# Kernel tuning notes

Hardware: AMD Instinct MI355X
Metric: run time of the kernel (lower is better)

The kernel has to match this reference:

```python
import jax, jax.numpy as jnp
import numpy as np
import math

D_MODEL = 1024
NUM_HEADS = 16
D_KV = 64
INNER = NUM_HEADS * D_KV
NUM_BUCKETS = 32
MAX_DISTANCE = 128


def _relative_position_bucket(relative_position, num_buckets=NUM_BUCKETS, max_distance=MAX_DISTANCE):
    # bidirectional T5 bucketing
    n = -relative_position
    num_buckets = num_buckets // 2
    ret = (n < 0).astype(jnp.int32) * num_buckets
    n = jnp.abs(n)
    max_exact = num_buckets // 2
    is_small = n < max_exact
    n_safe = jnp.maximum(n, 1).astype(jnp.float32)  # avoid log(0); masked by is_small
    val_if_large = max_exact + (
        jnp.log(n_safe / max_exact) / math.log(max_distance / max_exact) * (num_buckets - max_exact)
    ).astype(jnp.int32)
    val_if_large = jnp.minimum(val_if_large, num_buckets - 1)
    return jnp.where(is_small, n, val_if_large) + ret


def _position_bias(rel_emb, q_len, k_len):
    ctx = jnp.arange(q_len)[:, None]
    mem = jnp.arange(k_len)[None, :]
    buckets = _relative_position_bucket(mem - ctx)          # [q, k]
    values = rel_emb[buckets]                               # [q, k, H]
    return jnp.transpose(values, (2, 0, 1))[None]           # [1, H, q, k]


def setup_inputs() -> dict:
    key = jax.random.key(0)
    ks = jax.random.split(key, 6)
    B, S = 2, 2048
    scale = 1.0 / math.sqrt(D_MODEL)
    return {
        "hidden_states": jax.random.normal(ks[0], (B, S, D_MODEL), dtype=jnp.float32),
        "mask": jnp.zeros((B, 1, 1, S), dtype=jnp.float32),
        "Wq": jax.random.normal(ks[1], (D_MODEL, INNER), dtype=jnp.float32) * scale,
        "Wk": jax.random.normal(ks[2], (D_MODEL, INNER), dtype=jnp.float32) * scale,
        "Wv": jax.random.normal(ks[3], (D_MODEL, INNER), dtype=jnp.float32) * scale,
        "Wo": jax.random.normal(ks[4], (INNER, D_MODEL), dtype=jnp.float32) * scale,
        "rel_emb": jax.random.normal(ks[5], (NUM_BUCKETS, NUM_HEADS), dtype=jnp.float32),
    }


def reference(hidden_states, mask, Wq, Wk, Wv, Wo, rel_emb):
    B, S, _ = hidden_states.shape
    def split_heads(x):
        return jnp.transpose(x.reshape(B, -1, NUM_HEADS, D_KV), (0, 2, 1, 3))  # [B,H,S,d]
    q = split_heads(hidden_states @ Wq)
    k = split_heads(hidden_states @ Wk)
    v = split_heads(hidden_states @ Wv)
    scores = jnp.einsum("bhqd,bhkd->bhqk", q, k)            # unscaled, T5-style
    position_bias = _position_bias(rel_emb, S, S)           # [1,H,S,S]
    scores = scores + position_bias + mask
    attn = jax.nn.softmax(scores, axis=-1)
    context = jnp.einsum("bhqk,bhkd->bhqd", attn, v)
    context = jnp.transpose(context, (0, 2, 1, 3)).reshape(B, S, INNER)
    output = context @ Wo
    return output, position_bias
```

## Files before the change

kernel.cpp:

```cpp
#include <hip/hip_runtime.h>
#include <cstdint>

#define AS1 __attribute__((address_space(1)))
#define AS3 __attribute__((address_space(3)))

typedef _Float16 half8 __attribute__((ext_vector_type(8)));
typedef _Float16 half4_t __attribute__((ext_vector_type(4)));
typedef float v4f __attribute__((ext_vector_type(4)));

__device__ __forceinline__ void async_ld16(const void* g, void* l) {
  __builtin_amdgcn_global_load_lds((const AS1 uint32_t*)g, (AS3 uint32_t*)l, 16, 0, 0);
}

__device__ __forceinline__ int t5_bucket(int delta) {
  int n = -delta;
  int ret = 0;
  if (n < 0) { ret = 16; n = -n; }
  if (n < 8) return n + ret;
  if (n >= 91) return 15 + ret;
  if ((n & (n - 1)) == 0) {
    int l = 31 - __clz(n);
    int v = 2 + 2 * l;
    return (v > 15 ? 15 : v) + ret;
  }
  int v = 8 + (int)(logf((float)n * 0.125f) * (8.0f / logf(16.0f)));
  return (v > 15 ? 15 : v) + ret;
}

__global__ void k_prep(const float* __restrict__ hs, const float* __restrict__ Wq,
                       const float* __restrict__ Wk, const float* __restrict__ Wv,
                       const float* __restrict__ Wo, _Float16* __restrict__ hsF,
                       _Float16* __restrict__ wqkvT, _Float16* __restrict__ woT) {
  const int tid = threadIdx.x;
  if (blockIdx.x < 4096) {
    int t = blockIdx.x * 256 + tid;
    float4 f = ((const float4*)hs)[t];
    half4_t h = {(_Float16)f.x, (_Float16)f.y, (_Float16)f.z, (_Float16)f.w};
    ((half4_t*)hsF)[t] = h;
    return;
  }
  __shared__ float tile[32][33];
  const int idx = blockIdx.x - 4096;
  const int z = idx >> 10, rem = idx & 1023;
  const float* src = (z == 0) ? Wq : (z == 1) ? Wk : (z == 2) ? Wv : Wo;
  _Float16* dst = (z < 3) ? (wqkvT + ((size_t)z << 20)) : woT;
  const int tx = tid & 31, ty = tid >> 5;
  const int bx = (rem & 31) * 32, by = (rem >> 5) * 32;
#pragma unroll
  for (int i = 0; i < 32; i += 8)
    tile[ty + i][tx] = src[(size_t)(by + ty + i) * 1024 + bx + tx];
  __syncthreads();
#pragma unroll
  for (int i = 0; i < 32; i += 8)
    dst[(size_t)(bx + ty + i) * 1024 + by + tx] = (_Float16)tile[tx][ty + i];
}

__global__ __launch_bounds__(256, 3) void k_gemm_qkv_bias(
    const _Float16* __restrict__ A, const _Float16* __restrict__ BT,
    _Float16* __restrict__ qkv, _Float16* __restrict__ vT,
    const float* __restrict__ rel, float* __restrict__ outb) {
  __shared__ __align__(16) _Float16 As[128 * 32];
  __shared__ __align__(16) _Float16 Bs[128 * 32];
  __shared__ float btab[256];
  const int tid = threadIdx.x;
  const int wave = tid >> 6, lane = tid & 63;
  const int l15 = lane & 15, quad = lane >> 4;
  const int m0 = blockIdx.y * 128, n0 = blockIdx.x * 128;
  const int wm = (wave >> 1) * 64, wn = (wave & 1) * 64;
  const int r0 = tid >> 2, c0 = (tid & 3) * 8;
  constexpr int K = 1024;

  const int bid = blockIdx.y * 24 + blockIdx.x;
  const bool do_bias = bid < 512;
  const int hB = bid >> 5;
  const int qoff = (bid & 31) * 64;
  float c_past = 0.f, c_fut = 0.f;
  if (do_bias) {
    btab[tid & 255] = rel[t5_bucket((tid & 255) - 128) * 16 + hB];
    c_past = rel[15 * 16 + hB];
    c_fut = rel[31 * 16 + hB];
  }

  v4f acc[4][4] = {};
  for (int k0 = 0; k0 < K; k0 += 32) {
    asm volatile("s_waitcnt lgkmcnt(0)\ns_barrier" ::: "memory");
    async_ld16(A + (size_t)(m0 + r0) * K + k0 + c0, (char*)As + (size_t)(wave * 64) * 16);
    async_ld16(A + (size_t)(m0 + 64 + r0) * K + k0 + c0,
               (char*)As + (size_t)(256 + wave * 64) * 16);
    async_ld16(BT + (size_t)(n0 + r0) * K + k0 + c0, (char*)Bs + (size_t)(wave * 64) * 16);
    async_ld16(BT + (size_t)(n0 + 64 + r0) * K + k0 + c0,
               (char*)Bs + (size_t)(256 + wave * 64) * 16);

    if (do_bias) {
      __builtin_amdgcn_sched_barrier(0);
      const int iter = k0 >> 5;
#pragma unroll
      for (int j = 0; j < 2; ++j) {
        int fi = iter * 512 + j * 256 + tid;
        int qr = qoff + (fi >> 8);
        int c = fi & 255;
        int k4 = ((c >> 4) << 5) + (c & 15);
        int kb = k4 << 2;
        float4 v;
        if (kb - qr >= 91) {
          v = make_float4(c_fut, c_fut, c_fut, c_fut);
        } else if (qr - kb - 3 >= 91) {
          v = make_float4(c_past, c_past, c_past, c_past);
        } else {
          v.x = btab[kb + 0 - qr + 128];
          v.y = btab[kb + 1 - qr + 128];
          v.z = btab[kb + 2 - qr + 128];
          v.w = btab[kb + 3 - qr + 128];
        }
        ((float4*)outb)[((size_t)hB * 2048 + qr) * 512 + k4] = v;
      }
      asm volatile("s_waitcnt vmcnt(2) lgkmcnt(0)\ns_barrier" ::: "memory");
    } else {
      asm volatile("s_waitcnt vmcnt(0) lgkmcnt(0)\ns_barrier" ::: "memory");
    }

    half8 af[4], bf[4];
#pragma unroll
    for (int mt = 0; mt < 4; ++mt)
      af[mt] = *(const half8*)(As + (wm + mt * 16 + l15) * 32 + quad * 8);
#pragma unroll
    for (int nt = 0; nt < 4; ++nt)
      bf[nt] = *(const half8*)(Bs + (wn + nt * 16 + l15) * 32 + quad * 8);
#pragma unroll
    for (int mt = 0; mt < 4; ++mt)
#pragma unroll
      for (int nt = 0; nt < 4; ++nt)
        acc[mt][nt] = __builtin_amdgcn_mfma_f32_16x16x32_f16(af[mt], bf[nt], acc[mt][nt], 0, 0, 0);
  }
  if (n0 >= 2048) {
#pragma unroll
    for (int mt = 0; mt < 4; ++mt)
#pragma unroll
      for (int nt = 0; nt < 4; ++nt) {
        int col = n0 + wn + nt * 16 + l15 - 2048;
        int row0 = m0 + wm + mt * 16 + quad * 4;
        int bb = row0 >> 11, s0 = row0 & 2047;
        half4_t hv = {(_Float16)acc[mt][nt][0], (_Float16)acc[mt][nt][1],
                      (_Float16)acc[mt][nt][2], (_Float16)acc[mt][nt][3]};
        *(half4_t*)(vT + ((size_t)bb * 1024 + col) * 2048 + s0) = hv;
      }
    return;
  }
#pragma unroll
  for (int mt = 0; mt < 4; ++mt)
#pragma unroll
    for (int nt = 0; nt < 4; ++nt)
#pragma unroll
      for (int r = 0; r < 4; ++r)
        qkv[(size_t)(m0 + wm + mt * 16 + quad * 4 + r) * 3072 + n0 + wn + nt * 16 + l15] =
            (_Float16)acc[mt][nt][r];
}

__global__ __launch_bounds__(256, 2) void k_gemm_n64(const _Float16* __restrict__ A,
                                                     const _Float16* __restrict__ BT,
                                                     float* __restrict__ C, int K, int ldc) {
  __shared__ __align__(16) _Float16 As[128 * 32];
  __shared__ __align__(16) _Float16 Bs[64 * 32];
  const int tid = threadIdx.x;
  const int wave = tid >> 6, lane = tid & 63;
  const int l15 = lane & 15, quad = lane >> 4;
  const int m0 = blockIdx.y * 128, n0 = blockIdx.x * 64;
  const int wm = (wave >> 1) * 64, wn = (wave & 1) * 32;
  const int r0 = tid >> 2, c0 = (tid & 3) * 8;
  v4f acc[4][2] = {};
  for (int k0 = 0; k0 < K; k0 += 32) {
    asm volatile("s_waitcnt lgkmcnt(0)\ns_barrier" ::: "memory");
    async_ld16(A + (size_t)(m0 + r0) * K + k0 + c0, (char*)As + (size_t)(wave * 64) * 16);
    async_ld16(A + (size_t)(m0 + 64 + r0) * K + k0 + c0,
               (char*)As + (size_t)(256 + wave * 64) * 16);
    async_ld16(BT + (size_t)(n0 + r0) * K + k0 + c0, (char*)Bs + (size_t)(wave * 64) * 16);
    asm volatile("s_waitcnt vmcnt(0) lgkmcnt(0)\ns_barrier" ::: "memory");
    half8 af[4], bf[2];
#pragma unroll
    for (int mt = 0; mt < 4; ++mt)
      af[mt] = *(const half8*)(As + (wm + mt * 16 + l15) * 32 + quad * 8);
#pragma unroll
    for (int nt = 0; nt < 2; ++nt)
      bf[nt] = *(const half8*)(Bs + (wn + nt * 16 + l15) * 32 + quad * 8);
#pragma unroll
    for (int mt = 0; mt < 4; ++mt)
#pragma unroll
      for (int nt = 0; nt < 2; ++nt)
        acc[mt][nt] = __builtin_amdgcn_mfma_f32_16x16x32_f16(af[mt], bf[nt], acc[mt][nt], 0, 0, 0);
  }
#pragma unroll
  for (int mt = 0; mt < 4; ++mt)
#pragma unroll
    for (int nt = 0; nt < 2; ++nt)
#pragma unroll
      for (int r = 0; r < 4; ++r)
        C[(size_t)(m0 + wm + mt * 16 + quad * 4 + r) * ldc + n0 + wn + nt * 16 + l15] =
            acc[mt][nt][r];
}

__global__ __launch_bounds__(512, 4) void k_attn(const _Float16* __restrict__ qkv,
                                                 const _Float16* __restrict__ vT,
                                                 const float* __restrict__ mask,
                                                 const float* __restrict__ rel,
                                                 _Float16* __restrict__ ctx,
                                                 float* __restrict__ outb) {
  constexpr int S = 2048, LD = 3072;
  __shared__ __align__(16) _Float16 Ks[2][64 * 72];
  __shared__ __align__(16) _Float16 VT[2][64 * 72];
  __shared__ __align__(16) _Float16 Psh[128 * 72];
  __shared__ float btab[512];
  const int tid = threadIdx.x, wave = tid >> 6, lane = tid & 63;
  const int l15 = lane & 15, quad = lane >> 4;
  const int flat = blockIdx.x + 16 * (blockIdx.y + 16 * blockIdx.z);
  const int swz = (flat & 7) * 64 + (flat >> 3);
  const int q0 = (swz & 15) * 128, h = (swz >> 4) & 15, b = swz >> 8;

  btab[tid] = rel[t5_bucket((int)tid - 256) * 16 + h];
  const float c_past = rel[15 * 16 + h];
  const float c_fut = rel[31 * 16 + h];

  half8 bq[2];
  {
    const _Float16* qp = qkv + (size_t)(b * S + q0 + wave * 16 + l15) * LD + h * 64;
    bq[0] = *(const half8*)(qp + quad * 8);
    bq[1] = *(const half8*)(qp + 32 + quad * 8);
  }
  v4f o[4] = {};
  float mrun = -INFINITY;
  float lrun = 0.f;

  const int srow = tid >> 3, scol = (tid & 7) * 8;
  const _Float16* kg = qkv + (size_t)(b * S + srow) * LD + 1024 + h * 64 + scol;
  const _Float16* vg = vT + ((size_t)((b * 16 + h) * 64 + srow)) * S + scol;
  const float4* mkp = (const float4*)(mask + (size_t)b * S);

  const int qrow0 = q0 + b * 64;
  float4* const bias_base = (float4*)outb + ((size_t)h * 2048 + qrow0) * 512;

  {
    half8 kr = *(const half8*)(kg);
    half8 vr = *(const half8*)(vg);
    *(half8*)(&Ks[0][srow * 72 + scol]) = kr;
    *(half8*)(&VT[0][srow * 72 + scol]) = vr;
  }
  float4 mk[4];
#pragma unroll
  for (int mt = 0; mt < 4; ++mt) mk[mt] = mkp[mt * 4 + quad];
  __syncthreads();

  for (int kv0 = 0; kv0 < S; kv0 += 64) {
    const int buf = (kv0 >> 6) & 1;
    const bool more = (kv0 + 64) < S;
    half8 krn, vrn;
    float4 mkn[4];
    if (more) {
      krn = *(const half8*)(kg + (size_t)(kv0 + 64) * LD);
      vrn = *(const half8*)(vg + kv0 + 64);
#pragma unroll
      for (int mt = 0; mt < 4; ++mt) mkn[mt] = mkp[((kv0 + 64) >> 2) + mt * 4 + quad];
    }

    if (kv0 & 64) {
      const int diffw = kv0 - qrow0;
      float4* dst = bias_base + (kv0 >> 2);
      if (diffw >= 154) {
        const float4 v = make_float4(c_fut, c_fut, c_fut, c_fut);
#pragma unroll
        for (int j = 0; j < 2; ++j) {
          int fi = j * 512 + tid;
          dst[(size_t)(fi >> 4) * 512 + (fi & 15)] = v;
        }
      } else if (diffw <= -154) {
        const float4 v = make_float4(c_past, c_past, c_past, c_past);
#pragma unroll
        for (int j = 0; j < 2; ++j) {
          int fi = j * 512 + tid;
          dst[(size_t)(fi >> 4) * 512 + (fi & 15)] = v;
        }
      } else {
#pragma unroll
        for (int j = 0; j < 2; ++j) {
          int fi = j * 512 + tid;
          int row = fi >> 4, c4 = fi & 15;
          int q = qrow0 + row, k = kv0 + c4 * 4;
          float4 v;
          if (k - q >= 91) {
            v = make_float4(c_fut, c_fut, c_fut, c_fut);
          } else if (q - k - 3 >= 91) {
            v = make_float4(c_past, c_past, c_past, c_past);
          } else {
            int bi = k - q + 256;
            v.x = btab[bi + 0];
            v.y = btab[bi + 1];
            v.z = btab[bi + 2];
            v.w = btab[bi + 3];
          }
          dst[(size_t)row * 512 + c4] = v;
        }
      }
    }

    const _Float16* KsB = &Ks[buf][0];
    const _Float16* VTB = &VT[buf][0];
    v4f sc[4] = {};
    __builtin_amdgcn_s_setprio(1);
#pragma unroll
    for (int kc = 0; kc < 2; ++kc)
#pragma unroll
      for (int mt = 0; mt < 4; ++mt) {
        half8 af = *(const half8*)(KsB + (mt * 16 + l15) * 72 + kc * 32 + quad * 8);
        sc[mt] = __builtin_amdgcn_mfma_f32_16x16x32_f16(af, bq[kc], sc[mt], 0, 0, 0);
      }
    __builtin_amdgcn_s_setprio(0);

    const int diff = kv0 - q0;
    const bool mixed = (diff >= -153) && (diff <= 217);
    const float cf = (diff >= 218) ? c_fut : c_past;
    v4f cm[4];
#pragma unroll
    for (int mt = 0; mt < 4; ++mt) {
      cm[mt][0] = mk[mt].x; cm[mt][1] = mk[mt].y; cm[mt][2] = mk[mt].z; cm[mt][3] = mk[mt].w;
      if (!mixed) {
        cm[mt][0] += cf; cm[mt][1] += cf; cm[mt][2] += cf; cm[mt][3] += cf;
      }
    }
    if (mixed) {
      const int qq = q0 + wave * 16 + l15;
#pragma unroll
      for (int mt = 0; mt < 4; ++mt) {
        int base = kv0 + mt * 16 + quad * 4 - qq + 256;
#pragma unroll
        for (int r = 0; r < 4; ++r) sc[mt][r] += btab[base + r] + cm[mt][r];
      }
    } else {
#pragma unroll
      for (int mt = 0; mt < 4; ++mt)
#pragma unroll
        for (int r = 0; r < 4; ++r) sc[mt][r] += cm[mt][r];
    }

    {
      v4f m4 = sc[0];
#pragma unroll
      for (int r = 0; r < 4; ++r) {
        m4[r] = fmaxf(m4[r], sc[1][r]);
        m4[r] = fmaxf(m4[r], sc[2][r]);
        m4[r] = fmaxf(m4[r], sc[3][r]);
      }
      float mx = fmaxf(fmaxf(m4[0], m4[1]), fmaxf(m4[2], m4[3]));
      mx = fmaxf(mx, __shfl_xor(mx, 16, 64));
      mx = fmaxf(mx, __shfl_xor(mx, 32, 64));
      if (!__all(mx <= mrun)) {
        float mnew = fmaxf(mrun, mx);
        float alpha = __expf(mrun - mnew);
        mrun = mnew;
        lrun *= alpha;
#pragma unroll
        for (int dt = 0; dt < 4; ++dt)
#pragma unroll
          for (int r = 0; r < 4; ++r) o[dt][r] *= alpha;
      }
      const float mcur = mrun;
      v4f s4 = {};
#pragma unroll
      for (int mt = 0; mt < 4; ++mt)
#pragma unroll
        for (int r = 0; r < 4; ++r) {
          float p = __expf(sc[mt][r] - mcur);
          sc[mt][r] = p;
          s4[r] += p;
        }
      float rs = (s4[0] + s4[1]) + (s4[2] + s4[3]);
      rs += __shfl_xor(rs, 16, 64);
      rs += __shfl_xor(rs, 32, 64);
      lrun += rs;
      const int prow = wave * 16 + l15;
#pragma unroll
      for (int mt = 0; mt < 4; ++mt) {
        half4_t ph = {(_Float16)sc[mt][0], (_Float16)sc[mt][1],
                      (_Float16)sc[mt][2], (_Float16)sc[mt][3]};
        *(half4_t*)(Psh + prow * 72 + mt * 16 + quad * 4) = ph;
      }
    }

    __builtin_amdgcn_s_setprio(1);
#pragma unroll
    for (int kc = 0; kc < 2; ++kc) {
      half8 bp = *(const half8*)(Psh + (wave * 16 + l15) * 72 + kc * 32 + quad * 8);
#pragma unroll
      for (int dt = 0; dt < 4; ++dt) {
        half8 av = *(const half8*)(VTB + (dt * 16 + l15) * 72 + kc * 32 + quad * 8);
        o[dt] = __builtin_amdgcn_mfma_f32_16x16x32_f16(av, bp, o[dt], 0, 0, 0);
      }
    }
    __builtin_amdgcn_s_setprio(0);

    if (more) {
      _Float16* Kn = &Ks[buf ^ 1][0];
      _Float16* Vn = &VT[buf ^ 1][0];
      *(half8*)(Kn + srow * 72 + scol) = krn;
      *(half8*)(Vn + srow * 72 + scol) = vrn;
      asm volatile("s_waitcnt lgkmcnt(0)\ns_barrier" ::: "memory");
#pragma unroll
      for (int mt = 0; mt < 4; ++mt) mk[mt] = mkn[mt];
    }
  }
  {
    float inv = 1.0f / lrun;
    const size_t token = (size_t)(b * S + q0 + wave * 16 + l15);
#pragma unroll
    for (int dt = 0; dt < 4; ++dt) {
      half4_t hv = {(_Float16)(o[dt][0] * inv), (_Float16)(o[dt][1] * inv),
                    (_Float16)(o[dt][2] * inv), (_Float16)(o[dt][3] * inv)};
      *(half4_t*)(ctx + token * 1024 + h * 64 + dt * 16 + quad * 4) = hv;
    }
  }
}

extern "C" void kernel_launch(void* const* d_in, const int* in_sizes, int n_in,
                              void* d_out, int out_size, void* d_ws, size_t ws_size,
                              hipStream_t stream) {
  const float* hs = (const float*)d_in[0];
  const float* mask = (const float*)d_in[1];
  const float* Wq = (const float*)d_in[2];
  const float* Wk = (const float*)d_in[3];
  const float* Wv = (const float*)d_in[4];
  const float* Wo = (const float*)d_in[5];
  const float* rel = (const float*)d_in[6];
  float* out = (float*)d_out;

  char* ws = (char*)d_ws;
  _Float16* hsF = (_Float16*)(ws);
  _Float16* wqkvT = (_Float16*)(ws + (8u << 20));
  _Float16* woT = (_Float16*)(ws + (14u << 20));
  _Float16* qkv = (_Float16*)(ws + (16u << 20));
  _Float16* ctx = (_Float16*)(ws + (40u << 20));
  _Float16* vT = (_Float16*)(ws + (48u << 20));

  k_prep<<<8192, 256, 0, stream>>>(hs, Wq, Wk, Wv, Wo, hsF, wqkvT, woT);

  k_gemm_qkv_bias<<<dim3(24, 32), 256, 0, stream>>>(hsF, wqkvT, qkv, vT, rel,
                                                    out + 4194304);
  k_attn<<<dim3(16, 16, 2), 512, 0, stream>>>(qkv, vT, mask, rel, ctx, out + 4194304);
  k_gemm_n64<<<dim3(16, 32), 256, 0, stream>>>(ctx, woT, out, 1024, 1024);
}
```

Before: 420.7 us.

## Double-buffer LDS tiles in QKV and output projection GEMMs

Both GEMM kernels now keep two LDS buffers for A and B tiles and prefetch the next K-slice via async global-to-LDS loads while MFMAs run on the current slice. This is meant to hide global load latency that was previously exposed by a wait-then-compute loop. It doubles LDS use per block, which may lower occupancy. The loop end no longer waits on lgkmcnt before the barrier, which risks overwriting a buffer still being read from LDS.

After: 420.3 us. Within noise of the previous version (-0.1%).

```diff
diff --git a/kernel.cpp b/kernel.cpp
--- a/kernel.cpp
+++ b/kernel.cpp
@@ -59,8 +59,8 @@
     const _Float16* __restrict__ A, const _Float16* __restrict__ BT,
     _Float16* __restrict__ qkv, _Float16* __restrict__ vT,
     const float* __restrict__ rel, float* __restrict__ outb) {
-  __shared__ __align__(16) _Float16 As[128 * 32];
-  __shared__ __align__(16) _Float16 Bs[128 * 32];
+  __shared__ __align__(16) _Float16 As[2][128 * 32];
+  __shared__ __align__(16) _Float16 Bs[2][128 * 32];
   __shared__ float btab[256];
   const int tid = threadIdx.x;
   const int wave = tid >> 6, lane = tid & 63;
@@ -81,19 +81,32 @@
     c_fut = rel[31 * 16 + hB];
   }
 
+  async_ld16(A + (size_t)(m0 + r0) * K + c0, (char*)As[0] + (size_t)(wave * 64) * 16);
+  async_ld16(A + (size_t)(m0 + 64 + r0) * K + c0,
+             (char*)As[0] + (size_t)(256 + wave * 64) * 16);
+  async_ld16(BT + (size_t)(n0 + r0) * K + c0, (char*)Bs[0] + (size_t)(wave * 64) * 16);
+  async_ld16(BT + (size_t)(n0 + 64 + r0) * K + c0,
+             (char*)Bs[0] + (size_t)(256 + wave * 64) * 16);
+  asm volatile("s_waitcnt vmcnt(0) lgkmcnt(0)\ns_barrier" ::: "memory");
+
   v4f acc[4][4] = {};
-  for (int k0 = 0; k0 < K; k0 += 32) {
-    asm volatile("s_waitcnt lgkmcnt(0)\ns_barrier" ::: "memory");
-    async_ld16(A + (size_t)(m0 + r0) * K + k0 + c0, (char*)As + (size_t)(wave * 64) * 16);
-    async_ld16(A + (size_t)(m0 + 64 + r0) * K + k0 + c0,
-               (char*)As + (size_t)(256 + wave * 64) * 16);
-    async_ld16(BT + (size_t)(n0 + r0) * K + k0 + c0, (char*)Bs + (size_t)(wave * 64) * 16);
-    async_ld16(BT + (size_t)(n0 + 64 + r0) * K + k0 + c0,
-               (char*)Bs + (size_t)(256 + wave * 64) * 16);
+  for (int iter = 0; iter < 32; ++iter) {
+    const int buf = iter & 1;
+    const int k0 = iter * 32;
+    if (iter < 31) {
+      const int kn = k0 + 32;
+      async_ld16(A + (size_t)(m0 + r0) * K + kn + c0,
+                 (char*)As[buf ^ 1] + (size_t)(wave * 64) * 16);
+      async_ld16(A + (size_t)(m0 + 64 + r0) * K + kn + c0,
+                 (char*)As[buf ^ 1] + (size_t)(256 + wave * 64) * 16);
+      async_ld16(BT + (size_t)(n0 + r0) * K + kn + c0,
+                 (char*)Bs[buf ^ 1] + (size_t)(wave * 64) * 16);
+      async_ld16(BT + (size_t)(n0 + 64 + r0) * K + kn + c0,
+                 (char*)Bs[buf ^ 1] + (size_t)(256 + wave * 64) * 16);
+    }
+    __builtin_amdgcn_sched_barrier(0);
 
     if (do_bias) {
-      __builtin_amdgcn_sched_barrier(0);
-      const int iter = k0 >> 5;
 #pragma unroll
       for (int j = 0; j < 2; ++j) {
         int fi = iter * 512 + j * 256 + tid;
@@ -114,24 +127,28 @@
         }
         ((float4*)outb)[((size_t)hB * 2048 + qr) * 512 + k4] = v;
       }
-      asm volatile("s_waitcnt vmcnt(2) lgkmcnt(0)\ns_barrier" ::: "memory");
-    } else {
-      asm volatile("s_waitcnt vmcnt(0) lgkmcnt(0)\ns_barrier" ::: "memory");
     }
 
     half8 af[4], bf[4];
 #pragma unroll
     for (int mt = 0; mt < 4; ++mt)
-      af[mt] = *(const half8*)(As + (wm + mt * 16 + l15) * 32 + quad * 8);
+      af[mt] = *(const half8*)(&As[buf][(wm + mt * 16 + l15) * 32 + quad * 8]);
 #pragma unroll
     for (int nt = 0; nt < 4; ++nt)
-      bf[nt] = *(const half8*)(Bs + (wn + nt * 16 + l15) * 32 + quad * 8);
+      bf[nt] = *(const half8*)(&Bs[buf][(wn + nt * 16 + l15) * 32 + quad * 8]);
 #pragma unroll
     for (int mt = 0; mt < 4; ++mt)
 #pragma unroll
       for (int nt = 0; nt < 4; ++nt)
         acc[mt][nt] = __builtin_amdgcn_mfma_f32_16x16x32_f16(af[mt], bf[nt], acc[mt][nt], 0, 0, 0);
-  }
+
+    if (do_bias) {
+      asm volatile("s_waitcnt vmcnt(2)\ns_barrier" ::: "memory");
+    } else {
+      asm volatile("s_waitcnt vmcnt(0)\ns_barrier" ::: "memory");
+    }
+  }
+
   if (n0 >= 2048) {
 #pragma unroll
     for (int mt = 0; mt < 4; ++mt)
@@ -159,34 +176,47 @@
 __global__ __launch_bounds__(256, 2) void k_gemm_n64(const _Float16* __restrict__ A,
                                                      const _Float16* __restrict__ BT,
                                                      float* __restrict__ C, int K, int ldc) {
-  __shared__ __align__(16) _Float16 As[128 * 32];
-  __shared__ __align__(16) _Float16 Bs[64 * 32];
+  __shared__ __align__(16) _Float16 As[2][128 * 32];
+  __shared__ __align__(16) _Float16 Bs[2][64 * 32];
   const int tid = threadIdx.x;
   const int wave = tid >> 6, lane = tid & 63;
   const int l15 = lane & 15, quad = lane >> 4;
   const int m0 = blockIdx.y * 128, n0 = blockIdx.x * 64;
   const int wm = (wave >> 1) * 64, wn = (wave & 1) * 32;
   const int r0 = tid >> 2, c0 = (tid & 3) * 8;
+
+  async_ld16(A + (size_t)(m0 + r0) * K + c0, (char*)As[0] + (size_t)(wave * 64) * 16);
+  async_ld16(A + (size_t)(m0 + 64 + r0) * K + c0,
+             (char*)As[0] + (size_t)(256 + wave * 64) * 16);
+  async_ld16(BT + (size_t)(n0 + r0) * K + c0, (char*)Bs[0] + (size_t)(wave * 64) * 16);
+  asm volatile("s_waitcnt vmcnt(0) lgkmcnt(0)\ns_barrier" ::: "memory");
+
   v4f acc[4][2] = {};
-  for (int k0 = 0; k0 < K; k0 += 32) {
-    asm volatile("s_waitcnt lgkmcnt(0)\ns_barrier" ::: "memory");
-    async_ld16(A + (size_t)(m0 + r0) * K + k0 + c0, (char*)As + (size_t)(wave * 64) * 16);
-    async_ld16(A + (size_t)(m0 + 64 + r0) * K + k0 + c0,
-               (char*)As + (size_t)(256 + wave * 64) * 16);
-    async_ld16(BT + (size_t)(n0 + r0) * K + k0 + c0, (char*)Bs + (size_t)(wave * 64) * 16);
-    asm volatile("s_waitcnt vmcnt(0) lgkmcnt(0)\ns_barrier" ::: "memory");
+  const int iters = K >> 5;
+  for (int iter = 0; iter < iters; ++iter) {
+    const int buf = iter & 1;
+    if (iter < iters - 1) {
+      const int kn = iter * 32 + 32;
+      async_ld16(A + (size_t)(m0 + r0) * K + kn + c0,
+                 (char*)As[buf ^ 1] + (size_t)(wave * 64) * 16);
+      async_ld16(A + (size_t)(m0 + 64 + r0) * K + kn + c0,
+                 (char*)As[buf ^ 1] + (size_t)(256 + wave * 64) * 16);
+      async_ld16(BT + (size_t)(n0 + r0) * K + kn + c0,
+                 (char*)Bs[buf ^ 1] + (size_t)(wave * 64) * 16);
+    }
     half8 af[4], bf[2];
 #pragma unroll
     for (int mt = 0; mt < 4; ++mt)
-      af[mt] = *(const half8*)(As + (wm + mt * 16 + l15) * 32 + quad * 8);
+      af[mt] = *(const half8*)(&As[buf][(wm + mt * 16 + l15) * 32 + quad * 8]);
 #pragma unroll
     for (int nt = 0; nt < 2; ++nt)
-      bf[nt] = *(const half8*)(Bs + (wn + nt * 16 + l15) * 32 + quad * 8);
+      bf[nt] = *(const half8*)(&Bs[buf][(wn + nt * 16 + l15) * 32 + quad * 8]);
 #pragma unroll
     for (int mt = 0; mt < 4; ++mt)
 #pragma unroll
       for (int nt = 0; nt < 2; ++nt)
         acc[mt][nt] = __builtin_amdgcn_mfma_f32_16x16x32_f16(af[mt], bf[nt], acc[mt][nt], 0, 0, 0);
+    asm volatile("s_waitcnt vmcnt(0)\ns_barrier" ::: "memory");
   }
 #pragma unroll
   for (int mt = 0; mt < 4; ++mt)
```
